# Kernel optimization log

Hardware: AMD Instinct MI355X
Metric: run time of the kernel (lower is better)

The kernel has to match this reference:

```python
import jax, jax.numpy as jnp
import numpy as np

B, E, H, T = 16384, 1024, 16, 256  # batch, embed_dim, num_heads, tabular_dim
HD = E // H  # head_dim


def _mha_seq1(q, kv, Wqkv, bqkv, Wo, bo):
    """nn.MultiheadAttention with query/key/value of seq_len 1 (batch_first).
    q, kv: [B, E]; Wqkv: [3E, E]; bqkv: [3E]; Wo: [E, E]; bo: [E]."""
    Wq, Wk, Wv = jnp.split(Wqkv, 3, axis=0)
    bq, bk, bv = jnp.split(bqkv, 3)
    qp = (q @ Wq.T + bq).reshape(-1, H, HD)   # [B, H, HD]
    kp = (kv @ Wk.T + bk).reshape(-1, H, HD)
    vp = (kv @ Wv.T + bv).reshape(-1, H, HD)
    scores = jnp.sum(qp * kp, axis=-1, keepdims=True) * (1.0 / HD ** 0.5)  # [B, H, 1]
    w = jax.nn.softmax(scores, axis=-1)       # softmax over 1 key -> all ones
    out = (w * vp).reshape(-1, E)             # [B, E]
    return out @ Wo.T + bo


def setup_inputs() -> dict:
    key = jax.random.key(0)
    ks = jax.random.split(key, 16)
    s_e = 1.0 / E ** 0.5
    s_t = 1.0 / T ** 0.5
    return {
        "text_features": jax.random.normal(ks[0], (B, E), jnp.float32),
        "ecg_features": jax.random.normal(ks[1], (B, E), jnp.float32),
        "tabular_features": jax.random.normal(ks[2], (B, T), jnp.float32),
        "Wc_text": jax.random.uniform(ks[3], (E, T), jnp.float32, -s_t, s_t),
        "bc_text": jax.random.uniform(ks[4], (E,), jnp.float32, -s_t, s_t),
        "Wc_ecg": jax.random.uniform(ks[5], (E, T), jnp.float32, -s_t, s_t),
        "bc_ecg": jax.random.uniform(ks[6], (E,), jnp.float32, -s_t, s_t),
        "Wqkv_a": jax.random.uniform(ks[7], (3 * E, E), jnp.float32, -s_e, s_e),
        "bqkv_a": jnp.zeros((3 * E,), jnp.float32),
        "Wo_a": jax.random.uniform(ks[8], (E, E), jnp.float32, -s_e, s_e),
        "bo_a": jnp.zeros((E,), jnp.float32),
        "Wqkv_b": jax.random.uniform(ks[9], (3 * E, E), jnp.float32, -s_e, s_e),
        "bqkv_b": jnp.zeros((3 * E,), jnp.float32),
        "Wo_b": jax.random.uniform(ks[10], (E, E), jnp.float32, -s_e, s_e),
        "bo_b": jnp.zeros((E,), jnp.float32),
    }


def reference(text_features, ecg_features, tabular_features,
              Wc_text, bc_text, Wc_ecg, bc_ecg,
              Wqkv_a, bqkv_a, Wo_a, bo_a,
              Wqkv_b, bqkv_b, Wo_b, bo_b):
    text_scale = jax.nn.sigmoid(tabular_features @ Wc_text.T + bc_text)
    ecg_scale = jax.nn.sigmoid(tabular_features @ Wc_ecg.T + bc_ecg)
    text_query = text_features * text_scale
    ecg_query = ecg_features * ecg_scale
    attn_a = _mha_seq1(text_query, ecg_features, Wqkv_a, bqkv_a, Wo_a, bo_a)
    attn_b = _mha_seq1(ecg_query, text_features, Wqkv_b, bqkv_b, Wo_b, bo_b)
    return jnp.concatenate([attn_a, attn_b], axis=-1)
```

## Files before the change

kernel.cpp:

```cpp
#include <hip/hip_runtime.h>
#include <hip/hip_bf16.h>
#include <stdint.h>

typedef __bf16 bf16_t;
typedef bf16_t bf16x8 __attribute__((ext_vector_type(8)));
typedef bf16_t bf16x4 __attribute__((ext_vector_type(4)));
typedef float  f32x4  __attribute__((ext_vector_type(4)));

#define E_DIM 1024
#define B_ROWS 16384

__device__ __forceinline__ void gload_lds16(const void* g, void* l) {
    __builtin_amdgcn_global_load_lds(
        (const __attribute__((address_space(1))) void*)g,
        (__attribute__((address_space(3))) void*)l,
        16, 0, 0);
}

__global__ __launch_bounds__(256) void prep_w_k(const float* __restrict__ Wqkv_a,
                                                const float* __restrict__ bqkv_a,
                                                const float* __restrict__ Wo_a,
                                                const float* __restrict__ bo_a,
                                                const float* __restrict__ Wqkv_b,
                                                const float* __restrict__ bqkv_b,
                                                const float* __restrict__ Wo_b,
                                                const float* __restrict__ bo_b,
                                                bf16_t* __restrict__ WoB,
                                                bf16_t* __restrict__ WvT,
                                                float* __restrict__ beff) {
    const size_t MAT = (size_t)E_DIM * E_DIM;
    __shared__ float t[64][65];
    int b = blockIdx.x;
    int tid = threadIdx.x;
    if (b < 2048) {
        const int n4 = (int)(MAT / 4);
        int i = b * 256 + tid;
        const float* src = (i < n4) ? Wo_a : Wo_b;
        int j = (i < n4) ? i : i - n4;
        f32x4 v = ((const f32x4*)src)[j];
        bf16x4 o;
        o[0] = (bf16_t)v[0]; o[1] = (bf16_t)v[1];
        o[2] = (bf16_t)v[2]; o[3] = (bf16_t)v[3];
        ((bf16x4*)WoB)[i] = o;
    } else if (b < 2560) {
        int x = b - 2048;
        int ms = x >> 8;
        const float* in = (ms ? Wqkv_b : Wqkv_a) + 2 * MAT;
        bf16_t* o = WvT + (size_t)ms * MAT;
        int bb = x & 255;
        int bx = bb & 15, by = bb >> 4;
        int j0 = by * 64, k0 = bx * 64;
#pragma unroll
        for (int p = 0; p < 4; ++p) {
            int u = tid + 256 * p;
            int r = u >> 4, c4 = u & 15;
            f32x4 v = *(const f32x4*)(in + (size_t)(j0 + r) * E_DIM + k0 + c4 * 4);
            t[r][c4 * 4 + 0] = v[0]; t[r][c4 * 4 + 1] = v[1];
            t[r][c4 * 4 + 2] = v[2]; t[r][c4 * 4 + 3] = v[3];
        }
        __syncthreads();
#pragma unroll
        for (int p = 0; p < 4; ++p) {
            int u = tid + 256 * p;
            int r = u >> 4, c4 = u & 15;
            bf16x4 ov;
            ov[0] = (bf16_t)t[c4 * 4 + 0][r];
            ov[1] = (bf16_t)t[c4 * 4 + 1][r];
            ov[2] = (bf16_t)t[c4 * 4 + 2][r];
            ov[3] = (bf16_t)t[c4 * 4 + 3][r];
            *(bf16x4*)(o + (size_t)(k0 + r) * E_DIM + j0 + c4 * 4) = ov;
        }
    } else {
        int idx = (b - 2560) * 4 + (tid >> 6);
        int lane = tid & 63;
        int sel = idx >> 10;
        int i = idx & 1023;
        const float* Wo = sel ? Wo_b : Wo_a;
        const float* bv = (sel ? bqkv_b : bqkv_a) + 2 * E_DIM;
        const float* bo = sel ? bo_b : bo_a;
        float s = 0.f;
        for (int j = lane; j < E_DIM; j += 64)
            s += Wo[(size_t)i * E_DIM + j] * bv[j];
#pragma unroll
        for (int o = 32; o > 0; o >>= 1) s += __shfl_down(s, o);
        if (lane == 0) beff[sel * E_DIM + i] = s + bo[i];
    }
}

__global__ __launch_bounds__(256, 2) void combo_k(const float* __restrict__ ecg,
                                                  const float* __restrict__ text,
                                                  bf16_t* __restrict__ Xb,
                                                  const bf16_t* __restrict__ WoB,
                                                  const bf16_t* __restrict__ WvT,
                                                  bf16_t* __restrict__ Weff) {
    const size_t MAT = (size_t)E_DIM * E_DIM;
    __shared__ __align__(16) bf16_t As[128][64];
    __shared__ __align__(16) bf16_t Bs[128][64];

    int b = blockIdx.x;
    int tid = threadIdx.x;

    if (b < 2048) {
        const int half = (B_ROWS * E_DIM) / 8;
        const int total = 2 * half;
        const int stride = 2048 * 256;
        for (int i = b * 256 + tid; i < total; i += stride) {
            const float* src = (i < half) ? ecg : text;
            int j = (i < half) ? i : i - half;
            f32x4 lo = ((const f32x4*)src)[2 * j];
            f32x4 hi = ((const f32x4*)src)[2 * j + 1];
            bf16x8 v;
            v[0] = (bf16_t)lo[0]; v[1] = (bf16_t)lo[1]; v[2] = (bf16_t)lo[2]; v[3] = (bf16_t)lo[3];
            v[4] = (bf16_t)hi[0]; v[5] = (bf16_t)hi[1]; v[6] = (bf16_t)hi[2]; v[7] = (bf16_t)hi[3];
            ((bf16x8*)Xb)[i] = v;
        }
        return;
    }

    int bid = b - 2048;
    int ms = bid >> 6;
    int t  = bid & 63;
    int mt = t >> 3, nt = t & 7;
    const bf16_t* A  = WoB + (size_t)ms * MAT;
    const bf16_t* Bm = WvT + (size_t)ms * MAT;
    bf16_t*       C  = Weff + (size_t)ms * MAT;
    int m0 = mt * 128, n0 = nt * 128;

    int lane = tid & 63;
    int wid = tid >> 6;
    int wrow = (wid >> 1) * 64;
    int wcol = (wid & 1) * 64;
    int cl = lane & 15;
    int rg = lane >> 4;

    f32x4 acc[4][4] = {};

    for (int kt = 0; kt < 16; ++kt) {
#pragma unroll
        for (int i = 0; i < 4; ++i) {
            int chunk = i * 256 + wid * 64 + lane;
            int row = chunk >> 3;
            int kk8 = (chunk & 7) * 8;
            char* la = (char*)(&As[0][0]) + (size_t)(i * 256 + wid * 64) * 16;
            char* lb = (char*)(&Bs[0][0]) + (size_t)(i * 256 + wid * 64) * 16;
            gload_lds16(A  + (size_t)(m0 + row) * E_DIM + kt * 64 + kk8, la);
            gload_lds16(Bm + (size_t)(n0 + row) * E_DIM + kt * 64 + kk8, lb);
        }
        __syncthreads();
#pragma unroll
        for (int ks = 0; ks < 2; ++ks) {
            int kk = ks * 32 + rg * 8;
            bf16x8 af[4], bq[4];
#pragma unroll
            for (int m = 0; m < 4; ++m) af[m] = *(const bf16x8*)(&As[wrow + m * 16 + cl][kk]);
#pragma unroll
            for (int n = 0; n < 4; ++n) bq[n] = *(const bf16x8*)(&Bs[wcol + n * 16 + cl][kk]);
#pragma unroll
            for (int m = 0; m < 4; ++m)
#pragma unroll
                for (int n = 0; n < 4; ++n)
                    acc[m][n] = __builtin_amdgcn_mfma_f32_16x16x32_bf16(af[m], bq[n], acc[m][n], 0, 0, 0);
        }
        __syncthreads();
    }

#pragma unroll
    for (int m = 0; m < 4; ++m) {
        int r = m0 + wrow + m * 16 + rg * 4;
#pragma unroll
        for (int n = 0; n < 4; ++n) {
            int c = n0 + wcol + n * 16 + cl;
#pragma unroll
            for (int j = 0; j < 4; ++j)
                C[(size_t)(r + j) * E_DIM + c] = (bf16_t)acc[m][n][j];
        }
    }
}

#define VMW(n) asm volatile("s_waitcnt vmcnt(" #n ")" ::: "memory")
#define BAR()  __builtin_amdgcn_s_barrier()

__global__ __launch_bounds__(512, 2) void main_gemm_256_k(const bf16_t* __restrict__ Xb,
                                                          const bf16_t* __restrict__ Weff,
                                                          const float* __restrict__ beff,
                                                          float* __restrict__ out) {
    const size_t MAT  = (size_t)E_DIM * E_DIM;
    const size_t XMAT = (size_t)B_ROWS * E_DIM;

    int bid = blockIdx.x;
    int wg = (bid & 7) * 64 + (bid >> 3);
    int nt = wg & 7;
    int mt = wg >> 3;
    int sel = nt >> 2;
    int n0 = (nt & 3) * 256;
    int m0 = mt * 256;

    const bf16_t* gA = Xb + (size_t)sel * XMAT + (size_t)m0 * E_DIM;
    const bf16_t* gB = Weff + (size_t)sel * MAT + (size_t)n0 * E_DIM;
    const float*  bb = beff + sel * E_DIM;

    __shared__ __align__(16) bf16_t sA[2][256 * 64];
    __shared__ __align__(16) bf16_t sB[2][256 * 64];

    int tid  = threadIdx.x;
    int lane = tid & 63;
    int wid  = tid >> 6;
    int wr = wid >> 2;
    int wc = wid & 3;
    int cl = lane & 15;
    int rg = lane >> 4;
    int wr16cl = wr * 16 + cl;
    int wc16cl = wc * 16 + cl;

    int c0 = tid, c1 = 512 + tid;
    int r0 = c0 >> 3, r1 = c1 >> 3;
    int go0 = r0 * E_DIM + (((c0 & 7) * 8) ^ ((r0 & 7) << 3));
    int go1 = r1 * E_DIM + (((c1 & 7) * 8) ^ ((r1 & 7) << 3));
    int ld0 = c0 * 8, ld1 = c1 * 8;

    int koff0 = (rg * 8) ^ ((cl & 7) << 3);
    int koff1 = (32 + rg * 8) ^ ((cl & 7) << 3);

    f32x4 acc[8][4] = {};
    bf16x8 af[4][2], bq[2][2];

#define STAGE_A(kt, h, prt) do { \
    gload_lds16(gA + (size_t)((h) * 128) * E_DIM + (kt) * 64 + go0, &sA[prt][(h) * 8192 + ld0]); \
    gload_lds16(gA + (size_t)((h) * 128) * E_DIM + (kt) * 64 + go1, &sA[prt][(h) * 8192 + ld1]); } while (0)
#define STAGE_B(kt, h, prt) do { \
    gload_lds16(gB + (size_t)((h) * 128) * E_DIM + (kt) * 64 + go0, &sB[prt][(h) * 8192 + ld0]); \
    gload_lds16(gB + (size_t)((h) * 128) * E_DIM + (kt) * 64 + go1, &sB[prt][(h) * 8192 + ld1]); } while (0)
#define RD_A(p, mh) do { _Pragma("unroll") for (int m = 0; m < 4; ++m) { \
    af[m][0] = *(const bf16x8*)(&sA[p][((mh) * 128 + m * 32 + wr16cl) * 64 + koff0]); \
    af[m][1] = *(const bf16x8*)(&sA[p][((mh) * 128 + m * 32 + wr16cl) * 64 + koff1]); } } while (0)
#define RD_B(p, nh) do { _Pragma("unroll") for (int n = 0; n < 2; ++n) { \
    bq[n][0] = *(const bf16x8*)(&sB[p][((nh) * 128 + n * 64 + wc16cl) * 64 + koff0]); \
    bq[n][1] = *(const bf16x8*)(&sB[p][((nh) * 128 + n * 64 + wc16cl) * 64 + koff1]); } } while (0)
#define MM(mh, nh) do { __builtin_amdgcn_s_setprio(1); \
    _Pragma("unroll") for (int m = 0; m < 4; ++m) _Pragma("unroll") for (int n = 0; n < 2; ++n) { \
        acc[(mh) * 4 + m][(nh) * 2 + n] = __builtin_amdgcn_mfma_f32_16x16x32_bf16(af[m][0], bq[n][0], acc[(mh) * 4 + m][(nh) * 2 + n], 0, 0, 0); \
        acc[(mh) * 4 + m][(nh) * 2 + n] = __builtin_amdgcn_mfma_f32_16x16x32_bf16(af[m][1], bq[n][1], acc[(mh) * 4 + m][(nh) * 2 + n], 0, 0, 0); } \
    __builtin_amdgcn_s_setprio(0); } while (0)

    STAGE_A(0, 0, 0); STAGE_B(0, 0, 0); STAGE_B(0, 1, 0); STAGE_A(0, 1, 0);
    VMW(4);
    BAR();

#pragma unroll
    for (int t = 0; t < 16; ++t) {
        const int p = t & 1, pn = p ^ 1;
        RD_A(p, 0); RD_B(p, 0);
        if (t < 15) { STAGE_A(t + 1, 0, pn); VMW(4); } else { VMW(2); }
        BAR();
        MM(0, 0);
        BAR();
        RD_B(p, 1);
        if (t < 15) { STAGE_B(t + 1, 0, pn); VMW(4); } else { VMW(0); }
        BAR();
        MM(0, 1);
        BAR();
        RD_A(p, 1);
        if (t < 15) STAGE_B(t + 1, 1, pn);
        BAR();
        MM(1, 1);
        BAR();
        RD_B(p, 0);
        if (t < 15) { STAGE_A(t + 1, 1, pn); VMW(4); }
        BAR();
        MM(1, 0);
        BAR();
    }

#pragma unroll
    for (int mi = 0; mi < 8; ++mi) {
        int r = m0 + mi * 32 + wr * 16 + rg * 4;
#pragma unroll
        for (int n = 0; n < 4; ++n) {
            int ch = n0 + n * 64 + wc16cl;
            float bias = bb[ch];
            size_t gc = (size_t)sel * E_DIM + ch;
#pragma unroll
            for (int j = 0; j < 4; ++j)
                out[(size_t)(r + j) * (2 * E_DIM) + gc] = acc[mi][n][j] + bias;
        }
    }
#undef STAGE_A
#undef STAGE_B
#undef RD_A
#undef RD_B
#undef MM
}

extern "C" void kernel_launch(void* const* d_in, const int* in_sizes, int n_in,
                              void* d_out, int out_size, void* d_ws, size_t ws_size,
                              hipStream_t stream) {
    const float* text   = (const float*)d_in[0];
    const float* ecg    = (const float*)d_in[1];
    const float* Wqkv_a = (const float*)d_in[7];
    const float* bqkv_a = (const float*)d_in[8];
    const float* Wo_a   = (const float*)d_in[9];
    const float* bo_a   = (const float*)d_in[10];
    const float* Wqkv_b = (const float*)d_in[11];
    const float* bqkv_b = (const float*)d_in[12];
    const float* Wo_b   = (const float*)d_in[13];
    const float* bo_b   = (const float*)d_in[14];

    const size_t MAT  = (size_t)E_DIM * E_DIM;
    const size_t XMAT = (size_t)B_ROWS * E_DIM;
    bf16_t* WoB  = (bf16_t*)d_ws;
    bf16_t* WvT  = WoB + 2 * MAT;
    bf16_t* Weff = WvT + 2 * MAT;
    float*  beff = (float*)(Weff + 2 * MAT);
    bf16_t* Xb   = (bf16_t*)(beff + 2 * E_DIM);

    prep_w_k<<<3072, 256, 0, stream>>>(Wqkv_a, bqkv_a, Wo_a, bo_a,
                                       Wqkv_b, bqkv_b, Wo_b, bo_b,
                                       WoB, WvT, beff);
    combo_k<<<2176, 256, 0, stream>>>(ecg, text, Xb, WoB, WvT, Weff);
    main_gemm_256_k<<<512, 512, 0, stream>>>(Xb, Weff, beff, (float*)d_out);
}
```

Measured before the change: 148.8 us.

## Fuse weight prep into combo kernel and restructure main GEMM warp tiling

Removes the separate prep kernel. The Wo·Wv weight-fold GEMM now reads fp32 weights directly, converting and transposing them into LDS on the fly, and runs in the same launch as the bias fold and the activation bf16 conversion. This cuts one kernel launch and the bf16 weight-staging round trip through global memory. The main GEMM switches to a 4x2 warp layout with 64x128 per-warp tiles and reorders its staged loads and waits. The fold GEMM gives up its global_load_lds path for register loads and scalar transposed LDS stores, which may add bank conflicts.

```diff
diff --git a/kernel.cpp b/kernel.cpp
--- a/kernel.cpp
+++ b/kernel.cpp
@@ -17,61 +17,111 @@
         16, 0, 0);
 }
 
-__global__ __launch_bounds__(256) void prep_w_k(const float* __restrict__ Wqkv_a,
-                                                const float* __restrict__ bqkv_a,
-                                                const float* __restrict__ Wo_a,
-                                                const float* __restrict__ bo_a,
-                                                const float* __restrict__ Wqkv_b,
-                                                const float* __restrict__ bqkv_b,
-                                                const float* __restrict__ Wo_b,
-                                                const float* __restrict__ bo_b,
-                                                bf16_t* __restrict__ WoB,
-                                                bf16_t* __restrict__ WvT,
-                                                float* __restrict__ beff) {
+__global__ __launch_bounds__(256, 2) void combo2_k(const float* __restrict__ ecg,
+                                                   const float* __restrict__ text,
+                                                   const float* __restrict__ Wqkv_a,
+                                                   const float* __restrict__ bqkv_a,
+                                                   const float* __restrict__ Wo_a,
+                                                   const float* __restrict__ bo_a,
+                                                   const float* __restrict__ Wqkv_b,
+                                                   const float* __restrict__ bqkv_b,
+                                                   const float* __restrict__ Wo_b,
+                                                   const float* __restrict__ bo_b,
+                                                   bf16_t* __restrict__ Xb,
+                                                   bf16_t* __restrict__ Weff,
+                                                   float* __restrict__ beff) {
     const size_t MAT = (size_t)E_DIM * E_DIM;
-    __shared__ float t[64][65];
+    __shared__ __align__(16) bf16_t As[128][64];
+    __shared__ __align__(16) bf16_t Bs[128][64];
+
     int b = blockIdx.x;
     int tid = threadIdx.x;
-    if (b < 2048) {
-        const int n4 = (int)(MAT / 4);
-        int i = b * 256 + tid;
-        const float* src = (i < n4) ? Wo_a : Wo_b;
-        int j = (i < n4) ? i : i - n4;
-        f32x4 v = ((const f32x4*)src)[j];
-        bf16x4 o;
-        o[0] = (bf16_t)v[0]; o[1] = (bf16_t)v[1];
-        o[2] = (bf16_t)v[2]; o[3] = (bf16_t)v[3];
-        ((bf16x4*)WoB)[i] = o;
-    } else if (b < 2560) {
-        int x = b - 2048;
-        int ms = x >> 8;
-        const float* in = (ms ? Wqkv_b : Wqkv_a) + 2 * MAT;
-        bf16_t* o = WvT + (size_t)ms * MAT;
-        int bb = x & 255;
-        int bx = bb & 15, by = bb >> 4;
-        int j0 = by * 64, k0 = bx * 64;
-#pragma unroll
-        for (int p = 0; p < 4; ++p) {
-            int u = tid + 256 * p;
-            int r = u >> 4, c4 = u & 15;
-            f32x4 v = *(const f32x4*)(in + (size_t)(j0 + r) * E_DIM + k0 + c4 * 4);
-            t[r][c4 * 4 + 0] = v[0]; t[r][c4 * 4 + 1] = v[1];
-            t[r][c4 * 4 + 2] = v[2]; t[r][c4 * 4 + 3] = v[3];
-        }
-        __syncthreads();
-#pragma unroll
-        for (int p = 0; p < 4; ++p) {
-            int u = tid + 256 * p;
-            int r = u >> 4, c4 = u & 15;
-            bf16x4 ov;
-            ov[0] = (bf16_t)t[c4 * 4 + 0][r];
-            ov[1] = (bf16_t)t[c4 * 4 + 1][r];
-            ov[2] = (bf16_t)t[c4 * 4 + 2][r];
-            ov[3] = (bf16_t)t[c4 * 4 + 3][r];
-            *(bf16x4*)(o + (size_t)(k0 + r) * E_DIM + j0 + c4 * 4) = ov;
-        }
-    } else {
-        int idx = (b - 2560) * 4 + (tid >> 6);
+
+    if (b < 128) {
+        int ms = b >> 6;
+        int t2 = b & 63;
+        int mt = t2 >> 3, nt2 = t2 & 7;
+        const float* Wo = ms ? Wo_b : Wo_a;
+        const float* Wv = (ms ? Wqkv_b : Wqkv_a) + 2 * MAT;
+        bf16_t* C = Weff + (size_t)ms * MAT;
+        int m0 = mt * 128, n0 = nt2 * 128;
+
+        int lane = tid & 63;
+        int wid = tid >> 6;
+        int wrow = (wid >> 1) * 64;
+        int wcol = (wid & 1) * 64;
+        int cl = lane & 15;
+        int rg = lane >> 4;
+
+        int ar = tid >> 1, ah = tid & 1;
+        const float* aptr = Wo + (size_t)(m0 + ar) * E_DIM + ah * 32;
+        int jr = tid >> 2, cq = tid & 3;
+        const float* bptr = Wv + (size_t)jr * E_DIM + n0 + cq * 32;
+
+        f32x4 acc[4][4] = {};
+
+        for (int kt = 0; kt < 16; ++kt) {
+#pragma unroll
+            for (int h = 0; h < 2; ++h) {
+                f32x4 pa[4], pb[4];
+#pragma unroll
+                for (int q = 0; q < 4; ++q)
+                    pa[q] = *(const f32x4*)(aptr + kt * 64 + h * 16 + 4 * q);
+#pragma unroll
+                for (int w = 0; w < 4; ++w)
+                    pb[w] = *(const f32x4*)(bptr + (size_t)(kt * 64) * E_DIM + h * 16 + 4 * w);
+                bf16x8 v0, v1;
+                v0[0] = (bf16_t)pa[0][0]; v0[1] = (bf16_t)pa[0][1];
+                v0[2] = (bf16_t)pa[0][2]; v0[3] = (bf16_t)pa[0][3];
+                v0[4] = (bf16_t)pa[1][0]; v0[5] = (bf16_t)pa[1][1];
+                v0[6] = (bf16_t)pa[1][2]; v0[7] = (bf16_t)pa[1][3];
+                v1[0] = (bf16_t)pa[2][0]; v1[1] = (bf16_t)pa[2][1];
+                v1[2] = (bf16_t)pa[2][2]; v1[3] = (bf16_t)pa[2][3];
+                v1[4] = (bf16_t)pa[3][0]; v1[5] = (bf16_t)pa[3][1];
+                v1[6] = (bf16_t)pa[3][2]; v1[7] = (bf16_t)pa[3][3];
+                *(bf16x8*)(&As[ar][ah * 32 + h * 16]) = v0;
+                *(bf16x8*)(&As[ar][ah * 32 + h * 16 + 8]) = v1;
+#pragma unroll
+                for (int w = 0; w < 4; ++w) {
+#pragma unroll
+                    for (int e = 0; e < 4; ++e)
+                        Bs[cq * 32 + (h * 4 + w) * 4 + e][jr] = (bf16_t)pb[w][e];
+                }
+            }
+            __syncthreads();
+#pragma unroll
+            for (int ks = 0; ks < 2; ++ks) {
+                int kk = ks * 32 + rg * 8;
+                bf16x8 af[4], bq[4];
+#pragma unroll
+                for (int m = 0; m < 4; ++m) af[m] = *(const bf16x8*)(&As[wrow + m * 16 + cl][kk]);
+#pragma unroll
+                for (int n = 0; n < 4; ++n) bq[n] = *(const bf16x8*)(&Bs[wcol + n * 16 + cl][kk]);
+#pragma unroll
+                for (int m = 0; m < 4; ++m)
+#pragma unroll
+                    for (int n = 0; n < 4; ++n)
+                        acc[m][n] = __builtin_amdgcn_mfma_f32_16x16x32_bf16(af[m], bq[n], acc[m][n], 0, 0, 0);
+            }
+            __syncthreads();
+        }
+
+#pragma unroll
+        for (int m = 0; m < 4; ++m) {
+            int r = m0 + wrow + m * 16 + rg * 4;
+#pragma unroll
+            for (int n = 0; n < 4; ++n) {
+                int c = n0 + wcol + n * 16 + cl;
+#pragma unroll
+                for (int j = 0; j < 4; ++j)
+                    C[(size_t)(r + j) * E_DIM + c] = (bf16_t)acc[m][n][j];
+            }
+        }
+        return;
+    }
+
+    if (b < 640) {
+        int idx = (b - 128) * 4 + (tid >> 6);
         int lane = tid & 63;
         int sel = idx >> 10;
         int i = idx & 1023;
@@ -84,95 +134,24 @@
 #pragma unroll
         for (int o = 32; o > 0; o >>= 1) s += __shfl_down(s, o);
         if (lane == 0) beff[sel * E_DIM + i] = s + bo[i];
-    }
-}
-
-__global__ __launch_bounds__(256, 2) void combo_k(const float* __restrict__ ecg,
-                                                  const float* __restrict__ text,
-                                                  bf16_t* __restrict__ Xb,
-                                                  const bf16_t* __restrict__ WoB,
-                                                  const bf16_t* __restrict__ WvT,
-                                                  bf16_t* __restrict__ Weff) {
-    const size_t MAT = (size_t)E_DIM * E_DIM;
-    __shared__ __align__(16) bf16_t As[128][64];
-    __shared__ __align__(16) bf16_t Bs[128][64];
-
-    int b = blockIdx.x;
-    int tid = threadIdx.x;
-
-    if (b < 2048) {
-        const int half = (B_ROWS * E_DIM) / 8;
-        const int total = 2 * half;
-        const int stride = 2048 * 256;
-        for (int i = b * 256 + tid; i < total; i += stride) {
-            const float* src = (i < half) ? ecg : text;
-            int j = (i < half) ? i : i - half;
+        return;
+    }
+
+    const int half = (B_ROWS * E_DIM) / 8;
+    const int total = 2 * half;
+    const int stride = 2048 * 512;
+    for (int i = (b - 640) * 512 + tid * 2; i < total; i += stride) {
+#pragma unroll
+        for (int u = 0; u < 2; ++u) {
+            int idx = i + u;
+            const float* src = (idx < half) ? ecg : text;
+            int j = (idx < half) ? idx : idx - half;
             f32x4 lo = ((const f32x4*)src)[2 * j];
             f32x4 hi = ((const f32x4*)src)[2 * j + 1];
             bf16x8 v;
             v[0] = (bf16_t)lo[0]; v[1] = (bf16_t)lo[1]; v[2] = (bf16_t)lo[2]; v[3] = (bf16_t)lo[3];
             v[4] = (bf16_t)hi[0]; v[5] = (bf16_t)hi[1]; v[6] = (bf16_t)hi[2]; v[7] = (bf16_t)hi[3];
-            ((bf16x8*)Xb)[i] = v;
-        }
-        return;
-    }
-
-    int bid = b - 2048;
-    int ms = bid >> 6;
-    int t  = bid & 63;
-    int mt = t >> 3, nt = t & 7;
-    const bf16_t* A  = WoB + (size_t)ms * MAT;
-    const bf16_t* Bm = WvT + (size_t)ms * MAT;
-    bf16_t*       C  = Weff + (size_t)ms * MAT;
-    int m0 = mt * 128, n0 = nt * 128;
-
-    int lane = tid & 63;
-    int wid = tid >> 6;
-    int wrow = (wid >> 1) * 64;
-    int wcol = (wid & 1) * 64;
-    int cl = lane & 15;
-    int rg = lane >> 4;
-
-    f32x4 acc[4][4] = {};
-
-    for (int kt = 0; kt < 16; ++kt) {
-#pragma unroll
-        for (int i = 0; i < 4; ++i) {
-            int chunk = i * 256 + wid * 64 + lane;
-            int row = chunk >> 3;
-            int kk8 = (chunk & 7) * 8;
-            char* la = (char*)(&As[0][0]) + (size_t)(i * 256 + wid * 64) * 16;
-            char* lb = (char*)(&Bs[0][0]) + (size_t)(i * 256 + wid * 64) * 16;
-            gload_lds16(A  + (size_t)(m0 + row) * E_DIM + kt * 64 + kk8, la);
-            gload_lds16(Bm + (size_t)(n0 + row) * E_DIM + kt * 64 + kk8, lb);
-        }
-        __syncthreads();
-#pragma unroll
-        for (int ks = 0; ks < 2; ++ks) {
-            int kk = ks * 32 + rg * 8;
-            bf16x8 af[4], bq[4];
-#pragma unroll
-            for (int m = 0; m < 4; ++m) af[m] = *(const bf16x8*)(&As[wrow + m * 16 + cl][kk]);
-#pragma unroll
-            for (int n = 0; n < 4; ++n) bq[n] = *(const bf16x8*)(&Bs[wcol + n * 16 + cl][kk]);
-#pragma unroll
-            for (int m = 0; m < 4; ++m)
-#pragma unroll
-                for (int n = 0; n < 4; ++n)
-                    acc[m][n] = __builtin_amdgcn_mfma_f32_16x16x32_bf16(af[m], bq[n], acc[m][n], 0, 0, 0);
-        }
-        __syncthreads();
-    }
-
-#pragma unroll
-    for (int m = 0; m < 4; ++m) {
-        int r = m0 + wrow + m * 16 + rg * 4;
-#pragma unroll
-        for (int n = 0; n < 4; ++n) {
-            int c = n0 + wcol + n * 16 + cl;
-#pragma unroll
-            for (int j = 0; j < 4; ++j)
-                C[(size_t)(r + j) * E_DIM + c] = (bf16_t)acc[m][n][j];
+            ((bf16x8*)Xb)[idx] = v;
         }
     }
 }
@@ -180,10 +159,10 @@
 #define VMW(n) asm volatile("s_waitcnt vmcnt(" #n ")" ::: "memory")
 #define BAR()  __builtin_amdgcn_s_barrier()
 
-__global__ __launch_bounds__(512, 2) void main_gemm_256_k(const bf16_t* __restrict__ Xb,
-                                                          const bf16_t* __restrict__ Weff,
-                                                          const float* __restrict__ beff,
-                                                          float* __restrict__ out) {
+__global__ __launch_bounds__(512, 2) void main_gemm_v2_k(const bf16_t* __restrict__ Xb,
+                                                         const bf16_t* __restrict__ Weff,
+                                                         const float* __restrict__ beff,
+                                                         float* __restrict__ out) {
     const size_t MAT  = (size_t)E_DIM * E_DIM;
     const size_t XMAT = (size_t)B_ROWS * E_DIM;
 
@@ -205,12 +184,10 @@
     int tid  = threadIdx.x;
     int lane = tid & 63;
     int wid  = tid >> 6;
-    int wr = wid >> 2;
-    int wc = wid & 3;
+    int wr = wid >> 1;
+    int wc = wid & 1;
     int cl = lane & 15;
     int rg = lane >> 4;
-    int wr16cl = wr * 16 + cl;
-    int wc16cl = wc * 16 + cl;
 
     int c0 = tid, c1 = 512 + tid;
     int r0 = c0 >> 3, r1 = c1 >> 3;
@@ -221,8 +198,8 @@
     int koff0 = (rg * 8) ^ ((cl & 7) << 3);
     int koff1 = (32 + rg * 8) ^ ((cl & 7) << 3);
 
-    f32x4 acc[8][4] = {};
-    bf16x8 af[4][2], bq[2][2];
+    f32x4 acc[4][8] = {};
+    bf16x8 af[4], bq[4];
 
 #define STAGE_A(kt, h, prt) do { \
     gload_lds16(gA + (size_t)((h) * 128) * E_DIM + (kt) * 64 + go0, &sA[prt][(h) * 8192 + ld0]); \
@@ -230,58 +207,55 @@
 #define STAGE_B(kt, h, prt) do { \
     gload_lds16(gB + (size_t)((h) * 128) * E_DIM + (kt) * 64 + go0, &sB[prt][(h) * 8192 + ld0]); \
     gload_lds16(gB + (size_t)((h) * 128) * E_DIM + (kt) * 64 + go1, &sB[prt][(h) * 8192 + ld1]); } while (0)
-#define RD_A(p, mh) do { _Pragma("unroll") for (int m = 0; m < 4; ++m) { \
-    af[m][0] = *(const bf16x8*)(&sA[p][((mh) * 128 + m * 32 + wr16cl) * 64 + koff0]); \
-    af[m][1] = *(const bf16x8*)(&sA[p][((mh) * 128 + m * 32 + wr16cl) * 64 + koff1]); } } while (0)
-#define RD_B(p, nh) do { _Pragma("unroll") for (int n = 0; n < 2; ++n) { \
-    bq[n][0] = *(const bf16x8*)(&sB[p][((nh) * 128 + n * 64 + wc16cl) * 64 + koff0]); \
-    bq[n][1] = *(const bf16x8*)(&sB[p][((nh) * 128 + n * 64 + wc16cl) * 64 + koff1]); } } while (0)
-#define MM(mh, nh) do { __builtin_amdgcn_s_setprio(1); \
-    _Pragma("unroll") for (int m = 0; m < 4; ++m) _Pragma("unroll") for (int n = 0; n < 2; ++n) { \
-        acc[(mh) * 4 + m][(nh) * 2 + n] = __builtin_amdgcn_mfma_f32_16x16x32_bf16(af[m][0], bq[n][0], acc[(mh) * 4 + m][(nh) * 2 + n], 0, 0, 0); \
-        acc[(mh) * 4 + m][(nh) * 2 + n] = __builtin_amdgcn_mfma_f32_16x16x32_bf16(af[m][1], bq[n][1], acc[(mh) * 4 + m][(nh) * 2 + n], 0, 0, 0); } \
+#define RD_A(p, KOFF) do { _Pragma("unroll") for (int m = 0; m < 4; ++m) \
+    af[m] = *(const bf16x8*)(&sA[p][(wr * 64 + m * 16 + cl) * 64 + (KOFF)]); } while (0)
+#define RD_B(p, nh, KOFF) do { _Pragma("unroll") for (int n = 0; n < 4; ++n) \
+    bq[n] = *(const bf16x8*)(&sB[p][((nh) * 128 + wc * 64 + n * 16 + cl) * 64 + (KOFF)]); } while (0)
+#define MM(nh) do { __builtin_amdgcn_s_setprio(1); \
+    _Pragma("unroll") for (int m = 0; m < 4; ++m) _Pragma("unroll") for (int n = 0; n < 4; ++n) \
+        acc[m][(nh) * 4 + n] = __builtin_amdgcn_mfma_f32_16x16x32_bf16(af[m], bq[n], acc[m][(nh) * 4 + n], 0, 0, 0); \
     __builtin_amdgcn_s_setprio(0); } while (0)
 
-    STAGE_A(0, 0, 0); STAGE_B(0, 0, 0); STAGE_B(0, 1, 0); STAGE_A(0, 1, 0);
-    VMW(4);
+    STAGE_A(0, 0, 0); STAGE_A(0, 1, 0); STAGE_B(0, 0, 0); STAGE_B(0, 1, 0);
+    VMW(2);
     BAR();
 
 #pragma unroll
     for (int t = 0; t < 16; ++t) {
         const int p = t & 1, pn = p ^ 1;
-        RD_A(p, 0); RD_B(p, 0);
-        if (t < 15) { STAGE_A(t + 1, 0, pn); VMW(4); } else { VMW(2); }
-        BAR();
-        MM(0, 0);
-        BAR();
-        RD_B(p, 1);
-        if (t < 15) { STAGE_B(t + 1, 0, pn); VMW(4); } else { VMW(0); }
-        BAR();
-        MM(0, 1);
-        BAR();
-        RD_A(p, 1);
-        if (t < 15) STAGE_B(t + 1, 1, pn);
-        BAR();
-        MM(1, 1);
-        BAR();
-        RD_B(p, 0);
-        if (t < 15) { STAGE_A(t + 1, 1, pn); VMW(4); }
-        BAR();
-        MM(1, 0);
-        BAR();
-    }
-
-#pragma unroll
-    for (int mi = 0; mi < 8; ++mi) {
-        int r = m0 + mi * 32 + wr * 16 + rg * 4;
-#pragma unroll
-        for (int n = 0; n < 4; ++n) {
-            int ch = n0 + n * 64 + wc16cl;
+        RD_A(p, koff0); RD_B(p, 0, koff0);
+        if (t < 15) { STAGE_A(t + 1, 0, pn); VMW(2); } else { VMW(0); }
+        BAR();
+        MM(0);
+        BAR();
+        RD_B(p, 1, koff0);
+        if (t < 15) STAGE_A(t + 1, 1, pn);
+        BAR();
+        MM(1);
+        BAR();
+        RD_A(p, koff1); RD_B(p, 1, koff1);
+        if (t < 15) STAGE_B(t + 1, 0, pn);
+        BAR();
+        MM(1);
+        BAR();
+        RD_B(p, 0, koff1);
+        if (t < 15) { STAGE_B(t + 1, 1, pn); VMW(2); }
+        BAR();
+        MM(0);
+        BAR();
+    }
+
+#pragma unroll
+    for (int m = 0; m < 4; ++m) {
+        int r = m0 + wr * 64 + m * 16 + rg * 4;
+#pragma unroll
+        for (int ni = 0; ni < 8; ++ni) {
+            int ch = n0 + (ni >> 2) * 128 + wc * 64 + (ni & 3) * 16 + cl;
             float bias = bb[ch];
             size_t gc = (size_t)sel * E_DIM + ch;
 #pragma unroll
             for (int j = 0; j < 4; ++j)
-                out[(size_t)(r + j) * (2 * E_DIM) + gc] = acc[mi][n][j] + bias;
+                out[(size_t)(r + j) * (2 * E_DIM) + gc] = acc[m][ni][j] + bias;
         }
     }
 #undef STAGE_A
@@ -307,15 +281,13 @@
 
     const size_t MAT  = (size_t)E_DIM * E_DIM;
     const size_t XMAT = (size_t)B_ROWS * E_DIM;
-    bf16_t* WoB  = (bf16_t*)d_ws;
-    bf16_t* WvT  = WoB + 2 * MAT;
-    bf16_t* Weff = WvT + 2 * MAT;
+    bf16_t* Weff = (bf16_t*)d_ws;
     float*  beff = (float*)(Weff + 2 * MAT);
     bf16_t* Xb   = (bf16_t*)(beff + 2 * E_DIM);
 
-    prep_w_k<<<3072, 256, 0, stream>>>(Wqkv_a, bqkv_a, Wo_a, bo_a,
+    combo2_k<<<2688, 256, 0, stream>>>(ecg, text,
+                                       Wqkv_a, bqkv_a, Wo_a, bo_a,
                                        Wqkv_b, bqkv_b, Wo_b, bo_b,
-                                       WoB, WvT, beff);
-    combo_k<<<2176, 256, 0, stream>>>(ecg, text, Xb, WoB, WvT, Weff);
-    main_gemm_256_k<<<512, 512, 0, stream>>>(Xb, Weff, beff, (float*)d_out);
-}
+                                       Xb, Weff, beff);
+    main_gemm_v2_k<<<512, 512, 0, stream>>>(Xb, Weff, beff, (float*)d_out);
+}
```

Result: no change. 151.0 us (+1.5%).

## Restructure main GEMM warp tiling and reorder combo blocks so weight GEMM launches first

Applied to the files above, without the earlier changes.

Changes the main GEMM warp layout from a 2x4 grid of 16-row interleaved strips to a 4x2 grid of contiguous 64x128 warp tiles. The loop now runs k-halves in phases, staging A fully before B, with fewer fragment registers per phase. Separately, combo_k now places the weight-product GEMM blocks first so they get scheduled ahead of the conversion blocks. The new warp tile shape changes LDS read reuse (4 A and 4 B fragments per 16 MFMAs) and the wait/barrier schedule. This could help or hurt LDS bandwidth and latency hiding.

```diff
diff --git a/kernel.cpp b/kernel.cpp
--- a/kernel.cpp
+++ b/kernel.cpp
@@ -100,11 +100,11 @@
     int b = blockIdx.x;
     int tid = threadIdx.x;
 
-    if (b < 2048) {
+    if (b >= 128) {
         const int half = (B_ROWS * E_DIM) / 8;
         const int total = 2 * half;
         const int stride = 2048 * 256;
-        for (int i = b * 256 + tid; i < total; i += stride) {
+        for (int i = (b - 128) * 256 + tid; i < total; i += stride) {
             const float* src = (i < half) ? ecg : text;
             int j = (i < half) ? i : i - half;
             f32x4 lo = ((const f32x4*)src)[2 * j];
@@ -117,7 +117,7 @@
         return;
     }
 
-    int bid = b - 2048;
+    int bid = b;
     int ms = bid >> 6;
     int t  = bid & 63;
     int mt = t >> 3, nt = t & 7;
@@ -180,10 +180,10 @@
 #define VMW(n) asm volatile("s_waitcnt vmcnt(" #n ")" ::: "memory")
 #define BAR()  __builtin_amdgcn_s_barrier()
 
-__global__ __launch_bounds__(512, 2) void main_gemm_256_k(const bf16_t* __restrict__ Xb,
-                                                          const bf16_t* __restrict__ Weff,
-                                                          const float* __restrict__ beff,
-                                                          float* __restrict__ out) {
+__global__ __launch_bounds__(512, 2) void main_gemm_v2_k(const bf16_t* __restrict__ Xb,
+                                                         const bf16_t* __restrict__ Weff,
+                                                         const float* __restrict__ beff,
+                                                         float* __restrict__ out) {
     const size_t MAT  = (size_t)E_DIM * E_DIM;
     const size_t XMAT = (size_t)B_ROWS * E_DIM;
 
@@ -205,12 +205,10 @@
     int tid  = threadIdx.x;
     int lane = tid & 63;
     int wid  = tid >> 6;
-    int wr = wid >> 2;
-    int wc = wid & 3;
+    int wr = wid >> 1;
+    int wc = wid & 1;
     int cl = lane & 15;
     int rg = lane >> 4;
-    int wr16cl = wr * 16 + cl;
-    int wc16cl = wc * 16 + cl;
 
     int c0 = tid, c1 = 512 + tid;
     int r0 = c0 >> 3, r1 = c1 >> 3;
@@ -221,8 +219,8 @@
     int koff0 = (rg * 8) ^ ((cl & 7) << 3);
     int koff1 = (32 + rg * 8) ^ ((cl & 7) << 3);
 
-    f32x4 acc[8][4] = {};
-    bf16x8 af[4][2], bq[2][2];
+    f32x4 acc[4][8] = {};
+    bf16x8 af[4], bq[4];
 
 #define STAGE_A(kt, h, prt) do { \
     gload_lds16(gA + (size_t)((h) * 128) * E_DIM + (kt) * 64 + go0, &sA[prt][(h) * 8192 + ld0]); \
@@ -230,58 +228,55 @@
 #define STAGE_B(kt, h, prt) do { \
     gload_lds16(gB + (size_t)((h) * 128) * E_DIM + (kt) * 64 + go0, &sB[prt][(h) * 8192 + ld0]); \
     gload_lds16(gB + (size_t)((h) * 128) * E_DIM + (kt) * 64 + go1, &sB[prt][(h) * 8192 + ld1]); } while (0)
-#define RD_A(p, mh) do { _Pragma("unroll") for (int m = 0; m < 4; ++m) { \
-    af[m][0] = *(const bf16x8*)(&sA[p][((mh) * 128 + m * 32 + wr16cl) * 64 + koff0]); \
-    af[m][1] = *(const bf16x8*)(&sA[p][((mh) * 128 + m * 32 + wr16cl) * 64 + koff1]); } } while (0)
-#define RD_B(p, nh) do { _Pragma("unroll") for (int n = 0; n < 2; ++n) { \
-    bq[n][0] = *(const bf16x8*)(&sB[p][((nh) * 128 + n * 64 + wc16cl) * 64 + koff0]); \
-    bq[n][1] = *(const bf16x8*)(&sB[p][((nh) * 128 + n * 64 + wc16cl) * 64 + koff1]); } } while (0)
-#define MM(mh, nh) do { __builtin_amdgcn_s_setprio(1); \
-    _Pragma("unroll") for (int m = 0; m < 4; ++m) _Pragma("unroll") for (int n = 0; n < 2; ++n) { \
-        acc[(mh) * 4 + m][(nh) * 2 + n] = __builtin_amdgcn_mfma_f32_16x16x32_bf16(af[m][0], bq[n][0], acc[(mh) * 4 + m][(nh) * 2 + n], 0, 0, 0); \
-        acc[(mh) * 4 + m][(nh) * 2 + n] = __builtin_amdgcn_mfma_f32_16x16x32_bf16(af[m][1], bq[n][1], acc[(mh) * 4 + m][(nh) * 2 + n], 0, 0, 0); } \
+#define RD_A(p, KOFF) do { _Pragma("unroll") for (int m = 0; m < 4; ++m) \
+    af[m] = *(const bf16x8*)(&sA[p][(wr * 64 + m * 16 + cl) * 64 + (KOFF)]); } while (0)
+#define RD_B(p, nh, KOFF) do { _Pragma("unroll") for (int n = 0; n < 4; ++n) \
+    bq[n] = *(const bf16x8*)(&sB[p][((nh) * 128 + wc * 64 + n * 16 + cl) * 64 + (KOFF)]); } while (0)
+#define MM(nh) do { __builtin_amdgcn_s_setprio(1); \
+    _Pragma("unroll") for (int m = 0; m < 4; ++m) _Pragma("unroll") for (int n = 0; n < 4; ++n) \
+        acc[m][(nh) * 4 + n] = __builtin_amdgcn_mfma_f32_16x16x32_bf16(af[m], bq[n], acc[m][(nh) * 4 + n], 0, 0, 0); \
     __builtin_amdgcn_s_setprio(0); } while (0)
 
-    STAGE_A(0, 0, 0); STAGE_B(0, 0, 0); STAGE_B(0, 1, 0); STAGE_A(0, 1, 0);
-    VMW(4);
+    STAGE_A(0, 0, 0); STAGE_A(0, 1, 0); STAGE_B(0, 0, 0); STAGE_B(0, 1, 0);
+    VMW(2);
     BAR();
 
 #pragma unroll
     for (int t = 0; t < 16; ++t) {
         const int p = t & 1, pn = p ^ 1;
-        RD_A(p, 0); RD_B(p, 0);
-        if (t < 15) { STAGE_A(t + 1, 0, pn); VMW(4); } else { VMW(2); }
-        BAR();
-        MM(0, 0);
-        BAR();
-        RD_B(p, 1);
-        if (t < 15) { STAGE_B(t + 1, 0, pn); VMW(4); } else { VMW(0); }
-        BAR();
-        MM(0, 1);
-        BAR();
-        RD_A(p, 1);
-        if (t < 15) STAGE_B(t + 1, 1, pn);
-        BAR();
-        MM(1, 1);
-        BAR();
-        RD_B(p, 0);
-        if (t < 15) { STAGE_A(t + 1, 1, pn); VMW(4); }
-        BAR();
-        MM(1, 0);
-        BAR();
-    }
-
-#pragma unroll
-    for (int mi = 0; mi < 8; ++mi) {
-        int r = m0 + mi * 32 + wr * 16 + rg * 4;
-#pragma unroll
-        for (int n = 0; n < 4; ++n) {
-            int ch = n0 + n * 64 + wc16cl;
+        RD_A(p, koff0); RD_B(p, 0, koff0);
+        if (t < 15) { STAGE_A(t + 1, 0, pn); VMW(2); } else { VMW(0); }
+        BAR();
+        MM(0);
+        BAR();
+        RD_B(p, 1, koff0);
+        if (t < 15) STAGE_A(t + 1, 1, pn);
+        BAR();
+        MM(1);
+        BAR();
+        RD_A(p, koff1); RD_B(p, 1, koff1);
+        if (t < 15) STAGE_B(t + 1, 0, pn);
+        BAR();
+        MM(1);
+        BAR();
+        RD_B(p, 0, koff1);
+        if (t < 15) { STAGE_B(t + 1, 1, pn); VMW(2); }
+        BAR();
+        MM(0);
+        BAR();
+    }
+
+#pragma unroll
+    for (int m = 0; m < 4; ++m) {
+        int r = m0 + wr * 64 + m * 16 + rg * 4;
+#pragma unroll
+        for (int ni = 0; ni < 8; ++ni) {
+            int ch = n0 + (ni >> 2) * 128 + wc * 64 + (ni & 3) * 16 + cl;
             float bias = bb[ch];
             size_t gc = (size_t)sel * E_DIM + ch;
 #pragma unroll
             for (int j = 0; j < 4; ++j)
-                out[(size_t)(r + j) * (2 * E_DIM) + gc] = acc[mi][n][j] + bias;
+                out[(size_t)(r + j) * (2 * E_DIM) + gc] = acc[m][ni][j] + bias;
         }
     }
 #undef STAGE_A
@@ -317,5 +312,5 @@
                                        Wqkv_b, bqkv_b, Wo_b, bo_b,
                                        WoB, WvT, beff);
     combo_k<<<2176, 256, 0, stream>>>(ecg, text, Xb, WoB, WvT, Weff);
-    main_gemm_256_k<<<512, 512, 0, stream>>>(Xb, Weff, beff, (float*)d_out);
-}
+    main_gemm_v2_k<<<512, 512, 0, stream>>>(Xb, Weff, beff, (float*)d_out);
+}
```

After: 135.4 us. 1.1x faster.
